# Kernel optimization log

Measured on AMD Instinct MI355X. Metric: run time of the kernel, lower is better.

Reference implementation:

```python
import jax, jax.numpy as jnp
import numpy as np

# Static config (matches init_kwargs / input_specs)
B, D, H, W, C = 1, 16, 56, 56, 128
NH = 4
WS = (8, 7, 7)            # window size (d, h, w)
SS = (4, 3, 3)            # shift size = window // 2
HID = 4 * C
L = WS[0] * WS[1] * WS[2]  # 392 tokens per window
SCALE = (C // NH) ** -0.5
TABLE = (2 * WS[0] - 1) * (2 * WS[1] - 1) * (2 * WS[2] - 1)  # 2535


def _rel_index_np(wd, wh, ww):
    # Faithful to VideoSwinWindowAttention.get_relative_position_index
    yy, zz, xx = np.meshgrid(np.arange(ww), np.arange(wd), np.arange(wh))  # 'xy'
    coords = np.stack([zz, yy, xx], axis=0).reshape(3, -1)
    rc = coords[:, :, None] - coords[:, None, :]
    rc = rc.transpose(1, 2, 0)
    z = (rc[:, :, 0] + wd - 1) * (2 * wh - 1) * (2 * ww - 1)
    x = (rc[:, :, 1] + wh - 1) * (2 * ww - 1)
    y = rc[:, :, 2] + ww - 1
    return (z + x + y).astype(np.int32)  # (L, L)


def _partition_np(x, ws):
    b, d, h, w, c = x.shape
    x = x.reshape(b, d // ws[0], ws[0], h // ws[1], ws[1], w // ws[2], ws[2], c)
    x = x.transpose(0, 1, 3, 5, 2, 4, 6, 7)
    return x.reshape(-1, ws[0] * ws[1] * ws[2], c)


def _compute_mask_np(d, h, w, ws, ss):
    img = np.zeros((1, d, h, w, 1))
    cnt = 0
    for ds in (slice(-ws[0]), slice(-ws[0], -ss[0]), slice(-ss[0], None)):
        for hs in (slice(-ws[1]), slice(-ws[1], -ss[1]), slice(-ss[1], None)):
            for wsl in (slice(-ws[2]), slice(-ws[2], -ss[2]), slice(-ss[2], None)):
                img[:, ds, hs, wsl, :] = cnt
                cnt += 1
    mw = _partition_np(img, ws)[..., 0]  # (nW, L)
    am = mw[:, None, :] - mw[:, :, None]
    return np.where(am != 0, -100.0, 0.0).astype(np.float32)  # (nW, L, L)


REL_INDEX = jnp.asarray(_rel_index_np(*WS))            # (L, L) int32
ATTN_MASK = jnp.asarray(_compute_mask_np(D, H, W, WS, SS))  # (nW, L, L)


def window_partition(x, ws):
    b, d, h, w, c = x.shape
    x = x.reshape(b, d // ws[0], ws[0], h // ws[1], ws[1], w // ws[2], ws[2], c)
    x = x.transpose(0, 1, 3, 5, 2, 4, 6, 7)
    return x.reshape(-1, ws[0] * ws[1] * ws[2], c)


def window_reverse(win, ws, b, d, h, w):
    x = win.reshape(b, d // ws[0], h // ws[1], w // ws[2], ws[0], ws[1], ws[2], -1)
    x = x.transpose(0, 1, 4, 2, 5, 3, 6, 7)
    return x.reshape(b, d, h, w, -1)


def layer_norm(x, g, b, eps=1e-5):
    m = jnp.mean(x, axis=-1, keepdims=True)
    v = jnp.mean(jnp.square(x - m), axis=-1, keepdims=True)
    return (x - m) * jax.lax.rsqrt(v + eps) * g + b


def window_attention(xw, qkv_w, qkv_b, rpb, proj_w, proj_b, mask):
    bn = xw.shape[0]
    qkv = (xw @ qkv_w + qkv_b).reshape(bn, L, 3, NH, C // NH)
    q = qkv[:, :, 0].transpose(0, 2, 1, 3) * SCALE  # (bn, NH, L, hd)
    k = qkv[:, :, 1].transpose(0, 2, 1, 3)
    v = qkv[:, :, 2].transpose(0, 2, 1, 3)
    attn = jnp.einsum('bhld,bhmd->bhlm', q, k)
    bias = rpb[REL_INDEX.reshape(-1)].reshape(L, L, NH).transpose(2, 0, 1)
    attn = attn + bias[None]
    if mask is not None:
        nw = mask.shape[0]
        attn = attn.reshape(bn // nw, nw, NH, L, L) + mask[None, :, None]
        attn = attn.reshape(bn, NH, L, L)
    attn = jax.nn.softmax(attn, axis=-1)
    out = jnp.einsum('bhlm,bhmd->bhld', attn, v)
    out = out.transpose(0, 2, 1, 3).reshape(bn, L, C)
    return out @ proj_w + proj_b


def swin_block(x, p, shift, mask):
    shortcut = x
    x = layer_norm(x, p[0], p[1])
    if shift is not None:
        x = jnp.roll(x, (-shift[0], -shift[1], -shift[2]), axis=(1, 2, 3))
    xw = window_partition(x, WS)
    xw = window_attention(xw, p[2], p[3], p[4], p[5], p[6], mask)
    x = window_reverse(xw, WS, B, D, H, W)
    if shift is not None:
        x = jnp.roll(x, shift, axis=(1, 2, 3))
    x = shortcut + x
    y = layer_norm(x, p[7], p[8])
    y = jax.nn.gelu(y @ p[9] + p[10], approximate=False) @ p[11] + p[12]
    return x + y


def setup_inputs() -> dict:
    key = jax.random.key(0)
    ks = jax.random.split(key, 8)
    s = 0.02
    return {
        'x': jax.random.normal(ks[0], (B, D, H, W, C), jnp.float32),
        'ln1_g': jnp.ones((2, C), jnp.float32),
        'ln1_b': jnp.zeros((2, C), jnp.float32),
        'qkv_w': jax.random.normal(ks[1], (2, C, 3 * C), jnp.float32) * s,
        'qkv_b': jnp.zeros((2, 3 * C), jnp.float32),
        'rpb': jax.random.normal(ks[2], (2, TABLE, NH), jnp.float32) * s,
        'proj_w': jax.random.normal(ks[3], (2, C, C), jnp.float32) * s,
        'proj_b': jnp.zeros((2, C), jnp.float32),
        'ln2_g': jnp.ones((2, C), jnp.float32),
        'ln2_b': jnp.zeros((2, C), jnp.float32),
        'fc1_w': jax.random.normal(ks[4], (2, C, HID), jnp.float32) * s,
        'fc1_b': jnp.zeros((2, HID), jnp.float32),
        'fc2_w': jax.random.normal(ks[5], (2, HID, C), jnp.float32) * s,
        'fc2_b': jnp.zeros((2, C), jnp.float32),
    }


def reference(x, ln1_g, ln1_b, qkv_w, qkv_b, rpb, proj_w, proj_b,
              ln2_g, ln2_b, fc1_w, fc1_b, fc2_w, fc2_b):
    # Block 0: W-MSA (no shift, no mask). Block 1: SW-MSA (shift + mask).
    for i, (shift, mask) in enumerate(((None, None), (SS, ATTN_MASK))):
        p = (ln1_g[i], ln1_b[i], qkv_w[i], qkv_b[i], rpb[i], proj_w[i],
             proj_b[i], ln2_g[i], ln2_b[i], fc1_w[i], fc1_b[i], fc2_w[i], fc2_b[i])
        x = swin_block(x, p, shift, mask)
    return x
```

## Files before the change

kernel.cpp:

```cpp
#include <hip/hip_runtime.h>
#include <hip/hip_bf16.h>
#include <math.h>


#define NTOK 50176
#define CC   128
#define LL   392
#define NWIN 128
#define NHEAD 4
#define HDIM 32
#define QKSCALE 0.17677669529663687f
#define LOG2E   1.4426950408889634f

#define KOFF    0
#define VOFF    12544
#define POFF    25088
#define LDS_U16 33280

#define KTILE   12544

#define KADDR(row, g) (((row) << 5) + ((((g) ^ ((row) & 3) ^ (((row) >> 2) & 3))) << 3))
#define VADDR(d, k) (VOFF + (d)*392 + (k))

#define BM_PER_HEAD (13*392*16)
#define BM_TOTAL    (8*4*BM_PER_HEAD)

typedef unsigned short u16;
typedef unsigned int   u32;
typedef unsigned long long u64;
typedef __attribute__((ext_vector_type(8))) short short8;
typedef __attribute__((ext_vector_type(4))) float f32x4;
typedef __attribute__((ext_vector_type(2))) unsigned int u32x2;
typedef __attribute__((ext_vector_type(4))) unsigned int u32x4;

#define GLDS(gp, lp) __builtin_amdgcn_global_load_lds( \
    (const __attribute__((address_space(1))) void*)(gp), \
    (__attribute__((address_space(3))) void*)(lp), 16, 0, 0)

__device__ __forceinline__ float b2f_lo(u32 u){ return __uint_as_float(u<<16); }
__device__ __forceinline__ float b2f_hi(u32 u){ return __uint_as_float(u & 0xffff0000u); }
__device__ __forceinline__ u16 f2b(float f){
  __hip_bfloat16 h = __float2bfloat16(f);
  return *reinterpret_cast<u16*>(&h);
}
__device__ __forceinline__ u32 cvtpk(float lo, float hi){
  u32 r; asm("v_cvt_pk_bf16_f32 %0, %1, %2" : "=v"(r) : "v"(lo), "v"(hi)); return r;
}

__device__ __forceinline__ int row_to_pos(int r, int shifted){
  int w = r / LL, t = r - w*LL;
  int wd = w >> 6, wh = (w >> 3) & 7, ww = w & 7;
  int td = t / 49, rem = t - td*49, th = rem / 7, tw = rem - th*7;
  int d = wd*8 + td, h = wh*7 + th, x = ww*7 + tw;
  if (shifted){ d = (d+4)&15; h += 3; if (h>=56) h-=56; x += 3; if (x>=56) x-=56; }
  return (d*56 + h)*56 + x;
}

__device__ __forceinline__ int pos_to_row_sh(int p){
  int d = p / 3136, rem = p - d*3136, h = rem / 56, x = rem - h*56;
  d = (d + 12) & 15; h -= 3; if (h < 0) h += 56; x -= 3; if (x < 0) x += 56;
  int wd = d >> 3, td = d & 7;
  int wh = h / 7, th = h - wh*7, ww = x / 7, tw = x - ww*7;
  return (wd*64 + wh*8 + ww)*LL + td*49 + th*7 + tw;
}

__global__ __launch_bounds__(256) void ln_kernel(
    const float* __restrict__ xf, const float* __restrict__ g,
    const float* __restrict__ b, u16* __restrict__ out, int do_map, int shifted)
{
  int wave = threadIdx.x >> 6, lane = threadIdx.x & 63;
  int r = blockIdx.x*4 + wave;
  int pos = do_map ? row_to_pos(r, shifted) : r;
  long src = (long)pos * CC;
  float v0 = xf[src+lane], v1 = xf[src+64+lane];
  float s = v0+v1, ss = v0*v0 + v1*v1;
  #pragma unroll
  for (int o=32; o>0; o>>=1){ s += __shfl_xor(s,o); ss += __shfl_xor(ss,o); }
  float mean = s*(1.f/CC);
  float var  = ss*(1.f/CC) - mean*mean;
  float rstd = rsqrtf(var + 1e-5f);
  long dst = (long)r*CC;
  out[dst + lane]      = f2b((v0-mean)*rstd*g[lane]    + b[lane]);
  out[dst + 64 + lane] = f2b((v1-mean)*rstd*g[64+lane] + b[64+lane]);
}

__global__ __launch_bounds__(256) void wtall_kernel(
    const float* __restrict__ qkvw, const float* __restrict__ projw,
    const float* __restrict__ fc1w, const float* __restrict__ fc2w,
    u16* __restrict__ wts)
{
  int t = blockIdx.x*256 + threadIdx.x;
  int blk = t / 196608, r = t - blk*196608;
  const float* in; int Kd, Nd, off;
  if (r < 49152)      { in = qkvw + (size_t)blk*49152; Kd = 128; Nd = 384; off = r; }
  else if (r < 65536) { in = projw + (size_t)blk*16384; Kd = 128; Nd = 128; off = r - 49152; }
  else if (r < 131072){ in = fc1w + (size_t)blk*65536;  Kd = 128; Nd = 512; off = r - 65536; }
  else                { in = fc2w + (size_t)blk*65536;  Kd = 512; Nd = 128; off = r - 131072; }
  int n = off / Kd, k = off - n*Kd;
  wts[t] = f2b(in[k*Nd + n]);
}

__global__ __launch_bounds__(256) void biasm_kernel(
    const float* __restrict__ rpb, u32* __restrict__ bm, int total)
{
  int t = blockIdx.x*256 + threadIdx.x;
  if (t >= total) return;
  int jj = t & 15; int rest = t >> 4;
  int i  = rest % 392; rest /= 392;
  int s  = rest % 13;  rest /= 13;
  int h  = rest & 3;   int cls = rest >> 2;
  int tdi=i/49, rmi=i-tdi*49, thi=rmi/7, twi=rmi-thi*7;
  u32 pack = 0;
  #pragma unroll
  for (int half=0; half<2; half++){
    int j = s*32 + jj + half*16;
    float v = -1e30f;
    if (j < LL){
      int tdj=j/49, rmj=j-tdj*49, thj=rmj/7, twj=rmj-thj*7;
      int idx = (tdi-tdj)*169 + (thi-thj)*13 + (twi-twj) + 1267;
      v = rpb[idx*NHEAD + h];
      bool neq = ((cls&4) && ((tdi<4) != (tdj<4)))
              || ((cls&2) && ((thi<4) != (thj<4)))
              || ((cls&1) && ((twi<4) != (twj<4)));
      if (neq) v -= 100.f;
      v *= LOG2E;
    }
    pack |= ((u32)f2b(v)) << (16*half);
  }
  bm[t] = pack;
}

template<int KD, int EPI, int LNF>
__global__ __launch_bounds__(256) void mm_kernel(
    const u16* __restrict__ A, const u16* __restrict__ Wt, int ldw,
    const float* __restrict__ bias, u16* __restrict__ OutB, int ldo,
    float* __restrict__ OutF, const float* __restrict__ Res,
    const float* __restrict__ lng, const float* __restrict__ lnb,
    float scaleq, int shifted, int use_bias)
{
  __shared__ __align__(16) u16 As[128*32];
  __shared__ __align__(16) u16 Bs[128*32];
  const int tid = threadIdx.x, lane = tid & 63, wv = tid >> 6;
  const int quad = lane >> 4, l15 = lane & 15;
  const int rh = wv >> 1, ch = wv & 1;
  const int r0 = blockIdx.x * 128, n0 = blockIdx.y * 128;
  const int srow = lane >> 2, spart = (lane & 3) * 8;

  f32x4 acc[4][4] = {};

  for (int kt = 0; kt < KD/32; kt++){
    const int k0 = kt*32;
    #pragma unroll
    for (int t=0;t<2;t++){
      const int rowbase = wv*32 + t*16;
      GLDS(&A [(long)(r0 + rowbase + srow)*KD  + k0 + spart], &As[rowbase*32]);
      GLDS(&Wt[(long)(n0 + rowbase + srow)*ldw + k0 + spart], &Bs[rowbase*32]);
    }
    __syncthreads();
    short8 af[4], bf[4];
    #pragma unroll
    for (int rt=0;rt<4;rt++)
      af[rt] = *reinterpret_cast<const short8*>(&As[(rh*64 + rt*16 + l15)*32 + quad*8]);
    #pragma unroll
    for (int ct=0;ct<4;ct++)
      bf[ct] = *reinterpret_cast<const short8*>(&Bs[(ch*64 + ct*16 + l15)*32 + quad*8]);
    #pragma unroll
    for (int rt=0;rt<4;rt++)
      #pragma unroll
      for (int ct=0;ct<4;ct++)
        acc[rt][ct] = __builtin_amdgcn_mfma_f32_16x16x32_bf16(af[rt], bf[ct], acc[rt][ct], 0,0,0);
    __syncthreads();
  }

  if (EPI == 0){
    const int y = blockIdx.y;
    if (y == 0){
      #pragma unroll
      for (int rt=0;rt<4;rt++)
        #pragma unroll
        for (int rr=0;rr<4;rr++){
          const int row_g = r0 + rh*64 + rt*16 + quad*4 + rr;
          #pragma unroll
          for (int ct=0;ct<4;ct++){
            const int c = ch*64 + ct*16 + l15;
            float v = (acc[rt][ct][rr] + bias[c]) * scaleq;
            OutB[(long)row_g*128 + c] = f2b(v);
          }
        }
    } else if (y == 1){
      u16* Kreg = OutB + (size_t)NTOK*128;
      #pragma unroll
      for (int rt=0;rt<4;rt++)
        #pragma unroll
        for (int rr=0;rr<4;rr++){
          const int row_g = r0 + rh*64 + rt*16 + quad*4 + rr;
          const int wi = row_g / 392, key = row_g - wi*392;
          #pragma unroll
          for (int ct=0;ct<4;ct++){
            const int c = ch*64 + ct*16 + l15;
            const int hd = c >> 5, d = c & 31;
            float v = acc[rt][ct][rr] + bias[128 + c];
            Kreg[(size_t)(wi*4 + hd)*KTILE + KADDR(key, d>>3) + (d&7)] = f2b(v);
          }
        }
    } else {
      u16* Vreg = OutB + (size_t)NTOK*256;
      #pragma unroll
      for (int rt=0;rt<4;rt++){
        const int rbase = r0 + rh*64 + rt*16 + quad*4;
        const int wi = rbase / 392, key0 = rbase - wi*392;
        #pragma unroll
        for (int ct=0;ct<4;ct++){
          const int c = ch*64 + ct*16 + l15;
          const int hd = c >> 5, d = c & 31;
          const float bb = bias[256 + c];
          u32 lo = cvtpk(acc[rt][ct][0] + bb, acc[rt][ct][1] + bb);
          u32 hi = cvtpk(acc[rt][ct][2] + bb, acc[rt][ct][3] + bb);
          u64 pk = (u64)lo | ((u64)hi << 32);
          *reinterpret_cast<u64*>(&Vreg[(size_t)(wi*4 + hd)*KTILE + (size_t)d*392 + key0]) = pk;
        }
      }
    }
  } else if (LNF == 0){
    #pragma unroll
    for (int rt=0;rt<4;rt++){
      #pragma unroll
      for (int rr=0;rr<4;rr++){
        const int row_g = r0 + rh*64 + rt*16 + quad*4 + rr;
        long pos = 0;
        if (EPI == 2) pos = (long)row_to_pos(row_g, shifted) * CC;
        #pragma unroll
        for (int ct=0;ct<4;ct++){
          const int col_g = n0 + ch*64 + ct*16 + l15;
          float v = acc[rt][ct][rr];
          if (EPI == 1){
            v += bias[col_g];
            v = 0.5f*v*(1.f + erff(v*0.70710678118654752f));
            OutB[(long)row_g*ldo + col_g] = f2b(v);
          } else if (EPI == 2){
            OutF[pos + col_g] = Res[pos + col_g] + v + bias[col_g];
          } else {
            float o = OutF[(long)row_g*CC + col_g] + v;
            if (use_bias) o += bias[col_g];
            OutF[(long)row_g*CC + col_g] = o;
          }
        }
      }
    }
  } else {
    float* red = (float*)As;
    int pose[4][4];
    #pragma unroll
    for (int rt=0;rt<4;rt++){
      #pragma unroll
      for (int rr=0;rr<4;rr++){
        const int row_g = r0 + rh*64 + rt*16 + quad*4 + rr;
        int pos = (EPI == 2) ? row_to_pos(row_g, shifted) : row_g;
        pose[rt][rr] = pos;
        long pb = (long)pos * CC;
        float s = 0.f, ss = 0.f;
        #pragma unroll
        for (int ct=0;ct<4;ct++){
          const int col_g = n0 + ch*64 + ct*16 + l15;
          float v = acc[rt][ct][rr];
          float o;
          if (EPI == 2) o = Res[pb + col_g] + v + bias[col_g];
          else { o = OutF[pb + col_g] + v; if (use_bias) o += bias[col_g]; }
          OutF[pb + col_g] = o;
          acc[rt][ct][rr] = o;
          s += o; ss += o*o;
        }
        #pragma unroll
        for (int off=1; off<16; off<<=1){
          s  += __shfl_xor(s,  off);
          ss += __shfl_xor(ss, off);
        }
        if (l15 == 0){
          int rl = rh*64 + rt*16 + quad*4 + rr;
          red[rl*4 + ch*2]     = s;
          red[rl*4 + ch*2 + 1] = ss;
        }
      }
    }
    __syncthreads();
    #pragma unroll
    for (int rt=0;rt<4;rt++){
      #pragma unroll
      for (int rr=0;rr<4;rr++){
        const int rl = rh*64 + rt*16 + quad*4 + rr;
        float st  = red[rl*4]     + red[rl*4 + 2];
        float sst = red[rl*4 + 1] + red[rl*4 + 3];
        float mean = st*(1.f/128.f);
        float var  = sst*(1.f/128.f) - mean*mean;
        float rstd = rsqrtf(var + 1e-5f);
        long oidx;
        if (LNF == 1) oidx = (long)pose[rt][rr] * CC;
        else          oidx = (long)pos_to_row_sh(pose[rt][rr]) * CC;
        #pragma unroll
        for (int ct=0;ct<4;ct++){
          const int col_g = n0 + ch*64 + ct*16 + l15;
          float val = (acc[rt][ct][rr] - mean)*rstd*lng[col_g] + lnb[col_g];
          OutB[oidx + col_g] = f2b(val);
        }
      }
    }
  }
}

__global__ __launch_bounds__(512, 4) void attn_kernel(
    const u16* __restrict__ qkv, const u32* __restrict__ bm,
    u16* __restrict__ out, int shifted)
{
  __shared__ __align__(16) u16 lds[LDS_U16];

  const int w = blockIdx.x >> 2, head = blockIdx.x & 3;
  const int tid = threadIdx.x, lane = tid & 63, wave = tid >> 6;
  const int quad = lane >> 4, l15 = lane & 15;
  const int wd = w>>6, wh = (w>>3)&7, ww = w&7;
  const int cls = shifted ? (((wd!=0)?4:0) | ((wh==7)?2:0) | ((ww==7)?1:0)) : 0;
  const u32* __restrict__ bmh = bm + (size_t)(cls*NHEAD + head)*BM_PER_HEAD;
  const int pbase = POFF + wave*1024;
  const int swz = l15 & 7;
  const int prow = pbase + l15*64;
  const int q2 = quad >> 1, qh = (quad & 1) << 2;

  {
    const u16* Kg = qkv + (size_t)NTOK*128 + (size_t)(w*4+head)*KTILE;
    const u16* Vg = qkv + (size_t)NTOK*256 + (size_t)(w*4+head)*KTILE;
    #pragma unroll
    for (int n = 0; n < 3; n++){
      GLDS(Kg + n*4096 + wave*512 + (lane<<3), &lds[KOFF + n*4096 + wave*512]);
      GLDS(Vg + n*4096 + wave*512 + (lane<<3), &lds[VOFF + n*4096 + wave*512]);
    }
    if (tid < 32){
      GLDS(Kg + 12288 + (lane<<3), &lds[KOFF + 12288]);
      GLDS(Vg + 12288 + (lane<<3), &lds[VOFF + 12288]);
    }
  }
  __syncthreads();

  for (int qt = wave; qt < 25; qt += 8){
    int iq = qt*16 + l15; if (iq > LL-1) iq = LL-1;
    short8 qf = *reinterpret_cast<const short8*>(
        &qkv[((size_t)(w*LL + iq))*128 + head*HDIM + quad*8]);

    float ls = 0.f;
    f32x4 oc0 = {0.f,0.f,0.f,0.f}, oc1 = {0.f,0.f,0.f,0.f};

    const int bmrow = iq*16 + quad*4;
    u32x4 bmA = *reinterpret_cast<const u32x4*>(&bmh[bmrow]);
    u32x4 bmB = *reinterpret_cast<const u32x4*>(&bmh[392*16 + bmrow]);
    short8 kf0 = *reinterpret_cast<const short8*>(&lds[KOFF + KADDR(     l15, quad)]);
    short8 kf1 = *reinterpret_cast<const short8*>(&lds[KOFF + KADDR(16 + l15, quad)]);
    short8 kf2 = *reinterpret_cast<const short8*>(&lds[KOFF + KADDR(32 + l15, quad)]);
    short8 kf3 = *reinterpret_cast<const short8*>(&lds[KOFF + KADDR(48 + l15, quad)]);

    for (int it = 0; it < 6; it++){
      const int kb = it*64;
      u32x4 bmAn = {}, bmBn = {};
      short8 kn0 = {}, kn1 = {}, kn2 = {}, kn3 = {};
      if (it < 5){
        bmAn = *reinterpret_cast<const u32x4*>(&bmh[(2*it+2)*392*16 + bmrow]);
        bmBn = *reinterpret_cast<const u32x4*>(&bmh[(2*it+3)*392*16 + bmrow]);
        kn0 = *reinterpret_cast<const short8*>(&lds[KOFF + KADDR(kb + 64 + l15, quad)]);
        kn1 = *reinterpret_cast<const short8*>(&lds[KOFF + KADDR(kb + 80 + l15, quad)]);
        kn2 = *reinterpret_cast<const short8*>(&lds[KOFF + KADDR(kb + 96 + l15, quad)]);
        kn3 = *reinterpret_cast<const short8*>(&lds[KOFF + KADDR(kb +112 + l15, quad)]);
      } else {
        bmAn = *reinterpret_cast<const u32x4*>(&bmh[12*392*16 + bmrow]);
        kn0 = *reinterpret_cast<const short8*>(&lds[KOFF + KADDR(384 + (l15 & 7), quad)]);
        kn1 = kn0;
      }

      f32x4 z = {0.f,0.f,0.f,0.f};
      __builtin_amdgcn_s_setprio(1);
      f32x4 c0 = __builtin_amdgcn_mfma_f32_16x16x32_bf16(kf0, qf, z, 0,0,0);
      f32x4 c1 = __builtin_amdgcn_mfma_f32_16x16x32_bf16(kf1, qf, z, 0,0,0);
      f32x4 c2 = __builtin_amdgcn_mfma_f32_16x16x32_bf16(kf2, qf, z, 0,0,0);
      f32x4 c3 = __builtin_amdgcn_mfma_f32_16x16x32_bf16(kf3, qf, z, 0,0,0);
      __builtin_amdgcn_s_setprio(0);

      float p0[4], p1[4], p2[4], p3[4];
      #pragma unroll
      for (int r=0;r<4;r++){
        p0[r] = exp2f(c0[r] + b2f_lo(bmA[r]));
        p1[r] = exp2f(c1[r] + b2f_hi(bmA[r]));
        p2[r] = exp2f(c2[r] + b2f_lo(bmB[r]));
        p3[r] = exp2f(c3[r] + b2f_hi(bmB[r]));
        ls += (p0[r] + p1[r]) + (p2[r] + p3[r]);
      }

      u32x2 w0, w1, w2, w3;
      w0.x = cvtpk(p0[0], p0[1]); w0.y = cvtpk(p0[2], p0[3]);
      w1.x = cvtpk(p1[0], p1[1]); w1.y = cvtpk(p1[2], p1[3]);
      w2.x = cvtpk(p2[0], p2[1]); w2.y = cvtpk(p2[2], p2[3]);
      w3.x = cvtpk(p3[0], p3[1]); w3.y = cvtpk(p3[2], p3[3]);
      *reinterpret_cast<u32x2*>(&lds[prow + (((0 + q2) ^ swz) << 3) + qh]) = w0;
      *reinterpret_cast<u32x2*>(&lds[prow + (((2 + q2) ^ swz) << 3) + qh]) = w1;
      *reinterpret_cast<u32x2*>(&lds[prow + (((4 + q2) ^ swz) << 3) + qh]) = w2;
      *reinterpret_cast<u32x2*>(&lds[prow + (((6 + q2) ^ swz) << 3) + qh]) = w3;

      short8 pa0 = *reinterpret_cast<const short8*>(&lds[prow + (((quad    ) ^ swz) << 3)]);
      short8 pa1 = *reinterpret_cast<const short8*>(&lds[prow + (((quad + 4) ^ swz) << 3)]);
      short8 vb00 = *reinterpret_cast<const short8*>(&lds[VADDR(     l15, kb      + quad*8)]);
      short8 vb01 = *reinterpret_cast<const short8*>(&lds[VADDR(16 + l15, kb      + quad*8)]);
      short8 vb10 = *reinterpret_cast<const short8*>(&lds[VADDR(     l15, kb + 32 + quad*8)]);
      short8 vb11 = *reinterpret_cast<const short8*>(&lds[VADDR(16 + l15, kb + 32 + quad*8)]);
      __builtin_amdgcn_s_setprio(1);
      oc0 = __builtin_amdgcn_mfma_f32_16x16x32_bf16(pa0, vb00, oc0, 0,0,0);
      oc1 = __builtin_amdgcn_mfma_f32_16x16x32_bf16(pa0, vb01, oc1, 0,0,0);
      oc0 = __builtin_amdgcn_mfma_f32_16x16x32_bf16(pa1, vb10, oc0, 0,0,0);
      oc1 = __builtin_amdgcn_mfma_f32_16x16x32_bf16(pa1, vb11, oc1, 0,0,0);
      __builtin_amdgcn_s_setprio(0);

      bmA = bmAn; bmB = bmBn;
      kf0 = kn0; kf1 = kn1; kf2 = kn2; kf3 = kn3;
    }

    {
      f32x4 z = {0.f,0.f,0.f,0.f};
      f32x4 c0 = __builtin_amdgcn_mfma_f32_16x16x32_bf16(kf0, qf, z, 0,0,0);
      f32x4 c1 = __builtin_amdgcn_mfma_f32_16x16x32_bf16(kf1, qf, z, 0,0,0);
      float p0[4], p1[4];
      #pragma unroll
      for (int r=0;r<4;r++){
        p0[r] = exp2f(c0[r] + b2f_lo(bmA[r]));
        p1[r] = exp2f(c1[r] + b2f_hi(bmA[r]));
        ls += p0[r] + p1[r];
      }
      u32x2 w0, w1;
      w0.x = cvtpk(p0[0], p0[1]); w0.y = cvtpk(p0[2], p0[3]);
      w1.x = cvtpk(p1[0], p1[1]); w1.y = cvtpk(p1[2], p1[3]);
      *reinterpret_cast<u32x2*>(&lds[prow + (((0 + q2) ^ swz) << 3) + qh]) = w0;
      *reinterpret_cast<u32x2*>(&lds[prow + (((2 + q2) ^ swz) << 3) + qh]) = w1;
      short8 pa0 = *reinterpret_cast<const short8*>(&lds[prow + ((quad ^ swz) << 3)]);
      short8 vb0 = *reinterpret_cast<const short8*>(&lds[VADDR(     l15, 384)]);
      short8 vb1 = *reinterpret_cast<const short8*>(&lds[VADDR(16 + l15, 384)]);
      oc0 = __builtin_amdgcn_mfma_f32_16x16x32_bf16(pa0, vb0, oc0, 0,0,0);
      oc1 = __builtin_amdgcn_mfma_f32_16x16x32_bf16(pa0, vb1, oc1, 0,0,0);
    }

    ls += __shfl_xor(ls, 16);
    ls += __shfl_xor(ls, 32);
    float inv = 1.f / ls;
    #pragma unroll
    for (int r=0;r<4;r++){
      float invr = __shfl(inv, quad*4 + r);
      int i = qt*16 + quad*4 + r;
      if (i < LL){
        long o = ((long)(w*LL + i))*CC + head*HDIM;
        out[o + l15]      = f2b(oc0[r]*invr);
        out[o + 16 + l15] = f2b(oc1[r]*invr);
      }
    }
  }
}

extern "C" void kernel_launch(void* const* d_in, const int* in_sizes, int n_in,
                              void* d_out, int out_size, void* d_ws, size_t ws_size,
                              hipStream_t stream)
{
  const float* x     = (const float*)d_in[0];
  const float* ln1g  = (const float*)d_in[1];
  const float* ln1b  = (const float*)d_in[2];
  const float* qkvw  = (const float*)d_in[3];
  const float* qkvb  = (const float*)d_in[4];
  const float* rpb   = (const float*)d_in[5];
  const float* projw = (const float*)d_in[6];
  const float* projb = (const float*)d_in[7];
  const float* ln2g  = (const float*)d_in[8];
  const float* ln2b  = (const float*)d_in[9];
  const float* fc1w  = (const float*)d_in[10];
  const float* fc1b  = (const float*)d_in[11];
  const float* fc2w  = (const float*)d_in[12];
  const float* fc2b  = (const float*)d_in[13];
  float* outf = (float*)d_out;

  u16* buf1 = (u16*)d_ws;
  u16* bufq = buf1 + (size_t)NTOK*CC;
  u16* ln2o = bufq + (size_t)NTOK*256;
  u16* hid  = bufq + (size_t)NTOK*384;
  u16* wts  = hid  + (size_t)NTOK*512;
  u32* bm   = (u32*)(wts + 393216);

  wtall_kernel<<<1536, 256, 0, stream>>>(qkvw, projw, fc1w, fc2w, wts);

  for (int blk = 0; blk < 2; ++blk){
    const int sh = blk;
    const float* resid = (blk==0) ? x : outf;
    u16* wb = wts + (size_t)blk*196608;

    const int bmtot = (blk==0) ? 4*BM_PER_HEAD : BM_TOTAL;
    biasm_kernel<<<(bmtot+255)/256, 256, 0, stream>>>(
        rpb + (size_t)blk*2535*NHEAD, bm, bmtot);
    if (blk == 0)
      ln_kernel<<<NTOK/4, 256, 0, stream>>>(resid,
          ln1g, ln1b, buf1, 1, 0);
    mm_kernel<128,0,0><<<dim3(392,3), 256, 0, stream>>>(
        buf1, wb, 128, qkvb + blk*384, bufq, 128,
        nullptr, nullptr, nullptr, nullptr, QKSCALE*LOG2E, 0, 0);
    attn_kernel<<<NWIN*NHEAD, 512, 0, stream>>>(bufq, bm, buf1, sh);
    mm_kernel<128,2,1><<<dim3(392,1), 256, 0, stream>>>(
        buf1, wb+49152, 128, projb + blk*CC, ln2o, 0,
        outf, resid, ln2g + blk*CC, ln2b + blk*CC, 1.f, sh, 0);
    mm_kernel<128,1,0><<<dim3(392,4), 256, 0, stream>>>(
        ln2o, wb + 65536, 128,
        fc1b + blk*512, hid, 512,
        nullptr, nullptr, nullptr, nullptr, 1.f, 0, 0);
    if (blk == 0){
      mm_kernel<512,3,2><<<dim3(392,1), 256, 0, stream>>>(
          hid, wb + 131072, 512,
          fc2b, buf1, 0,
          outf, nullptr, ln1g + CC, ln1b + CC, 1.f, 0, 1);
    } else {
      mm_kernel<512,3,0><<<dim3(392,1), 256, 0, stream>>>(
          hid, wb + 131072, 512,
          fc2b + CC, nullptr, 0,
          outf, nullptr, nullptr, nullptr, 1.f, 0, 1);
    }
  }
}
```

Before: 415.4 us.

## Double-buffer LDS tiles in mm_kernel to overlap global loads with MFMA

Doubles the shared-memory A/B tiles in the GEMM kernel and prefetches the next K-slice via global-to-LDS loads while MFMAs run on the current buffer. The two __syncthreads per iteration become one explicit vmcnt wait plus barrier. The aim is to hide global load latency behind matrix work. The cost is twice the LDS per block, which may lower occupancy. It also relies on manual waitcnt semantics being correct for the LDS-direct loads.

```diff
diff --git a/kernel.cpp b/kernel.cpp
--- a/kernel.cpp
+++ b/kernel.cpp
@@ -138,39 +138,54 @@
     const float* __restrict__ lng, const float* __restrict__ lnb,
     float scaleq, int shifted, int use_bias)
 {
-  __shared__ __align__(16) u16 As[128*32];
-  __shared__ __align__(16) u16 Bs[128*32];
+  __shared__ __align__(16) u16 As[2*128*32];
+  __shared__ __align__(16) u16 Bs[2*128*32];
   const int tid = threadIdx.x, lane = tid & 63, wv = tid >> 6;
   const int quad = lane >> 4, l15 = lane & 15;
   const int rh = wv >> 1, ch = wv & 1;
   const int r0 = blockIdx.x * 128, n0 = blockIdx.y * 128;
   const int srow = lane >> 2, spart = (lane & 3) * 8;
+  const int nkt = KD/32;
 
   f32x4 acc[4][4] = {};
 
-  for (int kt = 0; kt < KD/32; kt++){
+  auto stage = [&](int kt, int bo){
     const int k0 = kt*32;
     #pragma unroll
     for (int t=0;t<2;t++){
       const int rowbase = wv*32 + t*16;
-      GLDS(&A [(long)(r0 + rowbase + srow)*KD  + k0 + spart], &As[rowbase*32]);
-      GLDS(&Wt[(long)(n0 + rowbase + srow)*ldw + k0 + spart], &Bs[rowbase*32]);
-    }
-    __syncthreads();
+      GLDS(&A [(long)(r0 + rowbase + srow)*KD  + k0 + spart], &As[bo + rowbase*32]);
+      GLDS(&Wt[(long)(n0 + rowbase + srow)*ldw + k0 + spart], &Bs[bo + rowbase*32]);
+    }
+  };
+  auto compute = [&](int bo){
     short8 af[4], bf[4];
     #pragma unroll
     for (int rt=0;rt<4;rt++)
-      af[rt] = *reinterpret_cast<const short8*>(&As[(rh*64 + rt*16 + l15)*32 + quad*8]);
+      af[rt] = *reinterpret_cast<const short8*>(&As[bo + (rh*64 + rt*16 + l15)*32 + quad*8]);
     #pragma unroll
     for (int ct=0;ct<4;ct++)
-      bf[ct] = *reinterpret_cast<const short8*>(&Bs[(ch*64 + ct*16 + l15)*32 + quad*8]);
+      bf[ct] = *reinterpret_cast<const short8*>(&Bs[bo + (ch*64 + ct*16 + l15)*32 + quad*8]);
     #pragma unroll
     for (int rt=0;rt<4;rt++)
       #pragma unroll
       for (int ct=0;ct<4;ct++)
         acc[rt][ct] = __builtin_amdgcn_mfma_f32_16x16x32_bf16(af[rt], bf[ct], acc[rt][ct], 0,0,0);
-    __syncthreads();
+  };
+
+  stage(0, 0);
+  asm volatile("s_waitcnt vmcnt(0)" ::: "memory");
+  __builtin_amdgcn_s_barrier();
+
+  int cur = 0;
+  for (int kt = 0; kt < nkt-1; kt++){
+    stage(kt+1, 4096 - cur);
+    compute(cur);
+    asm volatile("s_waitcnt vmcnt(0)" ::: "memory");
+    __builtin_amdgcn_s_barrier();
+    cur = 4096 - cur;
   }
+  compute(cur);
 
   if (EPI == 0){
     const int y = blockIdx.y;
```

Measured after the change: 415.7 us. No clear change (+0.1%).
